# Optimization experiments

Hardware: AMD Instinct MI355X
Metric: run time of the kernel (lower is better)

## Reference

```python
import jax, jax.numpy as jnp
import numpy as np

B, N = 16, 512


def _line_coords(n):
    # Discrete Fourier slice coordinates for all mValues (center=False, ridgelet=False).
    mu = n + n // 2 if n % 2 == 0 else n + 1
    p = 2 if n % 2 == 0 else n
    m = jnp.arange(mu)           # [mu]
    k = jnp.arange(n)            # [N]
    lt = (m < n)[:, None]        # m < N branch mask, [mu, 1]
    # m < N:  row = k,                 col = (k*m) % N
    # m >= N: row = (k*p*(m-N)) % N,   col = k
    row = jnp.where(lt, k[None, :], (k[None, :] * p * (m[:, None] - n)) % n)
    col = jnp.where(lt, (k[None, :] * m[:, None]) % n, k[None, :])
    return row, col  # each [mu, N] int32


def setup_inputs() -> dict:
    key = jax.random.key(0)
    return {"image": jax.random.normal(key, (B, N, N), dtype=jnp.float32)}


def reference(image):
    b, n, _ = image.shape
    row, col = _line_coords(n)                                   # [mu, N]
    dft = jnp.fft.fft2(image.astype(jnp.complex64), norm="ortho")  # [B, N, N] c64
    slices = dft[:, row, col]                                    # gather -> [B, mu, N]
    sino = jnp.fft.ifft(slices, norm="ortho")                    # [B, mu, N] c64
    # complex sinogram returned as stacked (real, imag) float channels
    return jnp.stack([sino.real, sino.imag], axis=-1)            # [B, mu, N, 2]
```

## Files before the change

### kernel.cpp

```cpp
#include <hip/hip_runtime.h>


#define NN 512
#define MU 768
#define MASK 511
#define SCALE 0.04419417382415922f

__global__ __launch_bounds__(256) void k_init(const float* __restrict__ img,
                                              float* __restrict__ A0,
                                              float* __restrict__ B0) {
  const int bx = blockIdx.x, b = blockIdx.y;
  const float* src = img + (size_t)b * NN * NN;
  if (bx < 32) {
    __shared__ float T1[64][65], T2[64][65], T3[64][65];
    const int xt = bx & 7, wt = bx >> 3;
    const int x0 = xt * 64, w0 = wt * 64, x3 = ((xt + 4) & 7) * 64;
    for (int idx = threadIdx.x; idx < 4096; idx += 256) {
      int rr = idx >> 6, cc = idx & 63;
      T1[rr][cc] = src[(x0 + rr) * NN + w0 + cc];
      T2[rr][cc] = src[(x0 + rr) * NN + w0 + 256 + cc];
      T3[rr][cc] = src[(x3 + rr) * NN + w0 + 256 + cc];
    }
    __syncthreads();
    float* dst = A0 + (size_t)b * (512 * NN);
    for (int idx = threadIdx.x; idx < 4096; idx += 256) {
      int wl = idx >> 6, xl = idx & 63;
      float t1 = T1[xl][wl];
      dst[(size_t)(w0 + wl) * NN + x0 + xl]       = t1 + T2[xl][wl];
      dst[(size_t)(256 + w0 + wl) * NN + x0 + xl] = t1 + T3[xl][wl];
    }
  } else {
    const int w0 = (bx - 32) * 32;
    const float4* s4 = (const float4*)src;
    float4* d4 = (float4*)(B0 + (size_t)b * (256 * NN));
    for (int it = 0; it < 16; ++it) {
      int flat = it * 256 + threadIdx.x;
      int row = w0 + (flat >> 7), col = flat & 127;
      float4 u = s4[row * 128 + col], v = s4[(row + 256) * 128 + col];
      u.x += v.x; u.y += v.y; u.z += v.z; u.w += v.w;
      d4[row * 128 + col] = u;
    }
  }
}

__global__ __launch_bounds__(512, 6) void k_pass1(const float* __restrict__ A0,
                                                  const float* __restrict__ B0,
                                                  float* __restrict__ A1,
                                                  float* __restrict__ B1) {
  __shared__ float L[16 * 512];
  const int bx = blockIdx.x, b = blockIdx.y;
  const int t = threadIdx.x;
  const bool isB = bx >= 32;
  const int c = isB ? 0 : (bx >> 4);
  const int w = isB ? (bx - 32) : (bx & 15);
  const float* in = isB ? (B0 + (size_t)b * 256 * NN) : (A0 + (size_t)b * 512 * NN);
  {
    const float4* s4 = (const float4*)in;
    float4* l4 = (float4*)L;
    const int pbase = c * 256 + w;
    for (int it = 0; it < 4; ++it) {
      int flat = it * 512 + t;
      int lrow = flat >> 7, col = flat & 127;
      l4[lrow * 128 + col] = s4[(pbase + 16 * lrow) * 128 + col];
    }
  }
  __syncthreads();
  const int g = t >> 7;
  const int x4 = (t & 127) * 4;
  float* outA = A1 + (size_t)b * 512 * NN;
  float* outB = B1 + (size_t)b * 256 * NN;
  for (int jj = 0; jj < 4; ++jj) {
    const int j = jj * 4 + g;
    const int C = isB ? (2 * j) : (c + 2 * j);
    float4 acc = {0.f, 0.f, 0.f, 0.f};
#pragma unroll
    for (int bb = 0; bb < 16; ++bb) {
      int base = (x4 - C * bb * 16) & MASK;
      float4 v = *(const float4*)&L[bb * 512 + base];
      acc.x += v.x; acc.y += v.y; acc.z += v.z; acc.w += v.w;
    }
    const int orow = isB ? (j * 16 + w) : (C * 16 + w);
    float* op = isB ? outB : outA;
    *(float4*)&op[(size_t)orow * NN + x4] = acc;
  }
}

__global__ __launch_bounds__(512, 6) void k_pass2(const float* __restrict__ A1,
                                                  const float* __restrict__ B1,
                                                  float2* __restrict__ out) {
  __shared__ float L[16 * 512];
  const int bx = blockIdx.x, b = blockIdx.y;
  const int t = threadIdx.x;
  const bool isB = bx >= 32;
  const int c = isB ? 2 * (bx - 32) : bx;
  const float* in = isB ? (B1 + (size_t)b * 256 * NN + (size_t)(bx - 32) * 16 * NN)
                        : (A1 + (size_t)b * 512 * NN + (size_t)c * 16 * NN);
#pragma unroll
  for (int bb = 0; bb < 16; ++bb) {
    float v = in[bb * 512 + t];
    L[bb * 512 + ((t + c * bb) & MASK)] = v;
  }
  __syncthreads();
  const int g = t >> 7;
  const int xq = (t & 127) << 2;
  float4 acc[4];
#pragma unroll
  for (int jj = 0; jj < 4; ++jj) acc[jj] = {0.f, 0.f, 0.f, 0.f};
#pragma unroll
  for (int bb = 0; bb < 16; ++bb) {
    const float* row = L + bb * 512;
    int base = (xq - 128 * g * bb) & MASK;
    const int step = (32 * bb) & MASK;
#pragma unroll
    for (int jj = 0; jj < 4; ++jj) {
      float4 v = *(const float4*)&row[base];
      acc[jj].x += v.x; acc[jj].y += v.y; acc[jj].z += v.z; acc[jj].w += v.w;
      base = (base - step) & MASK;
    }
  }
#pragma unroll
  for (int jj = 0; jj < 4; ++jj) {
    const int j = 4 * g + jj;
    const int m = isB ? (512 + (bx - 32) + 16 * j) : (c + 32 * j);
    float2* op = out + ((size_t)b * MU + m) * NN + xq;
    float4 a = acc[jj];
    op[0] = {a.x * SCALE, 0.f};
    op[1] = {a.y * SCALE, 0.f};
    op[2] = {a.z * SCALE, 0.f};
    op[3] = {a.w * SCALE, 0.f};
  }
}

#define TM 16
#define YT 16
#define LDS_STRIDE 516
__global__ __launch_bounds__(512) void drt_main(const float* __restrict__ img,
                                                float* __restrict__ out) {
  __shared__ float rows[YT * LDS_STRIDE];
  const int b = blockIdx.y;
  const int tile = blockIdx.x;
  const int t = threadIdx.x;
  const bool caseB = (tile >= 32);
  const int a0 = caseB ? (tile - 32) * TM : tile * TM;
  const float* __restrict__ src = img + (size_t)b * (NN * NN);
  const int slope0 = caseB ? (2 * a0) : a0;
  const int dslope = caseB ? 2 : 1;
  float acc[TM];
#pragma unroll
  for (int i = 0; i < TM; ++i) acc[i] = 0.0f;
  for (int y0 = 0; y0 < NN; y0 += YT) {
    __syncthreads();
    if (caseB) {
#pragma unroll
      for (int r = 0; r < YT; ++r) rows[r * LDS_STRIDE + t] = src[(y0 + r) * NN + t];
    } else {
#pragma unroll
      for (int rep = 0; rep < YT; ++rep) {
        int idx = rep * NN + t;
        int xx = idx >> 4, cc = idx & 15;
        rows[cc * LDS_STRIDE + xx] = src[xx * NN + y0 + cc];
      }
    }
    __syncthreads();
#pragma unroll 4
    for (int r = 0; r < YT; ++r) {
      const int v = y0 + r;
      int base = t - slope0 * v;
      const int step = dslope * v;
      const float* __restrict__ rowp = rows + r * LDS_STRIDE;
#pragma unroll
      for (int i = 0; i < TM; ++i) { acc[i] += rowp[base & MASK]; base -= step; }
    }
  }
  const int m = caseB ? (NN + a0) : a0;
  float2* outp = (float2*)out;
#pragma unroll
  for (int i = 0; i < TM; ++i) {
    float2 vv; vv.x = acc[i] * SCALE; vv.y = 0.0f;
    outp[((size_t)b * MU + (m + i)) * NN + t] = vv;
  }
}

extern "C" void kernel_launch(void* const* d_in, const int* in_sizes, int n_in,
                              void* d_out, int out_size, void* d_ws, size_t ws_size,
                              hipStream_t stream) {
  const float* img = (const float*)d_in[0];
  if (ws_size < (size_t)51 * 1024 * 1024) {
    drt_main<<<dim3(48, 16), dim3(512), 0, stream>>>(img, (float*)d_out);
    return;
  }
  float* W  = (float*)d_ws;
  float* A0 = W;
  float* A1 = W + 4194304;
  float* B0 = W + 8388608;
  float* B1 = W + 10485760;

  k_init <<<dim3(40, 16), dim3(256), 0, stream>>>(img, A0, B0);
  k_pass1<<<dim3(48, 16), dim3(512), 0, stream>>>(A0, B0, A1, B1);
  k_pass2<<<dim3(48, 16), dim3(512), 0, stream>>>(A1, B1, (float2*)d_out);
}
```

Before: 108.8 us.

## Fuse three DRT passes into one persistent kernel with fp16 intermediates

Merges the init, pass1 and pass2 kernels into a single persistent launch of 768 blocks that synchronises through atomic-counter grid barriers. The intermediate A/B buffers are stored in half precision to halve workspace traffic, and the final output uses nontemporal vector stores. This removes two kernel-launch gaps and cuts intermediate memory bandwidth. In exchange it loses precision in the intermediate sums, relies on all blocks being co-resident to avoid a barrier deadlock, adds a memset and an occupancy query on the host, and drops the workspace-free fallback.

```diff
diff --git a/kernel.cpp b/kernel.cpp
--- a/kernel.cpp
+++ b/kernel.cpp
@@ -1,10 +1,177 @@
 #include <hip/hip_runtime.h>
+#include <hip/hip_fp16.h>
 
 
 #define NN 512
 #define MU 768
 #define MASK 511
 #define SCALE 0.04419417382415922f
+#define NB 768
+
+typedef float v4f __attribute__((ext_vector_type(4)));
+
+union H8 { float4 f4; __half2 h2[4]; };
+union H4 { float2 f2; __half2 h2[2]; };
+
+__device__ __forceinline__ void gridbar(unsigned* cnt, unsigned target) {
+  __syncthreads();
+  if (threadIdx.x == 0) {
+    __threadfence();
+    atomicAdd(cnt, 1u);
+    while (__atomic_load_n(cnt, __ATOMIC_ACQUIRE) < target)
+      __builtin_amdgcn_s_sleep(8);
+    __threadfence();
+  }
+  __syncthreads();
+}
+
+__global__ __launch_bounds__(512, 6) void drt_fused(
+    const float* __restrict__ img, float2* __restrict__ out,
+    __half* __restrict__ A0, __half* __restrict__ B0,
+    __half* __restrict__ A1, __half* __restrict__ B1,
+    unsigned* __restrict__ bar) {
+  __shared__ float LDS[8320];
+  const int bid = blockIdx.x;
+  const int t = threadIdx.x;
+
+  if (bid < 512) {
+    const int b = bid >> 5, tile = bid & 31;
+    const int xt = tile & 7, wt = tile >> 3;
+    const int x0 = xt * 64, w0 = wt * 64, x3 = ((xt + 4) & 7) * 64;
+    const float* src = img + (size_t)b * NN * NN;
+    float* TA = LDS;
+    float* TB = LDS + 4160;
+    for (int idx = t; idx < 4096; idx += 512) {
+      int rr = idx >> 6, cc = idx & 63;
+      TA[rr * 65 + cc] = src[(x0 + rr) * NN + w0 + cc];
+      TB[rr * 65 + cc] = src[(x0 + rr) * NN + w0 + 256 + cc];
+    }
+    __syncthreads();
+    __half2* d = (__half2*)A0 + (size_t)b * 512 * 256;
+    for (int idx = t; idx < 2048; idx += 512) {
+      int wl = idx >> 5, xp = idx & 31;
+      float a0 = TA[(2 * xp) * 65 + wl] + TB[(2 * xp) * 65 + wl];
+      float a1 = TA[(2 * xp + 1) * 65 + wl] + TB[(2 * xp + 1) * 65 + wl];
+      d[(w0 + wl) * 256 + (x0 >> 1) + xp] = __float22half2_rn(make_float2(a0, a1));
+    }
+    __syncthreads();
+    for (int idx = t; idx < 4096; idx += 512) {
+      int rr = idx >> 6, cc = idx & 63;
+      TB[rr * 65 + cc] = src[(x3 + rr) * NN + w0 + 256 + cc];
+    }
+    __syncthreads();
+    for (int idx = t; idx < 2048; idx += 512) {
+      int wl = idx >> 5, xp = idx & 31;
+      float a0 = TA[(2 * xp) * 65 + wl] + TB[(2 * xp) * 65 + wl];
+      float a1 = TA[(2 * xp + 1) * 65 + wl] + TB[(2 * xp + 1) * 65 + wl];
+      d[(256 + w0 + wl) * 256 + (x0 >> 1) + xp] = __float22half2_rn(make_float2(a0, a1));
+    }
+  } else {
+    const int v = bid - 512, b = v >> 4, unit = v & 15;
+    const int w0 = unit * 16;
+    const float2* s2 = (const float2*)(img + (size_t)b * NN * NN);
+    __half2* d = (__half2*)B0 + (size_t)b * 256 * 256;
+    for (int it = 0; it < 8; ++it) {
+      int flat = it * 512 + t;
+      int row = w0 + (flat >> 8), cp = flat & 255;
+      float2 u = s2[row * 256 + cp], vv = s2[(row + 256) * 256 + cp];
+      d[row * 256 + cp] = __float22half2_rn(make_float2(u.x + vv.x, u.y + vv.y));
+    }
+  }
+
+  gridbar(bar, NB);
+
+  {
+    const int b = bid / 48, bx = bid - b * 48;
+    const bool isB = bx >= 32;
+    const int c = isB ? 0 : (bx >> 4);
+    const int w = isB ? (bx - 32) : (bx & 15);
+    const __half* in = isB ? (B0 + (size_t)b * 256 * NN) : (A0 + (size_t)b * 512 * NN);
+    const int pbase = c * 256 + w;
+    float* L = LDS;
+    const float4* s4 = (const float4*)in;
+    for (int it = 0; it < 2; ++it) {
+      int flat = it * 512 + t;
+      int lrow = flat >> 6, ch = flat & 63;
+      H8 u; u.f4 = s4[(size_t)(pbase + 16 * lrow) * 64 + ch];
+      float2 p0 = __half22float2(u.h2[0]), p1 = __half22float2(u.h2[1]);
+      float2 p2 = __half22float2(u.h2[2]), p3 = __half22float2(u.h2[3]);
+      float4* l4 = (float4*)&L[lrow * 512 + ch * 8];
+      l4[0] = make_float4(p0.x, p0.y, p1.x, p1.y);
+      l4[1] = make_float4(p2.x, p2.y, p3.x, p3.y);
+    }
+    __syncthreads();
+    const int g = t >> 7;
+    const int x4 = (t & 127) * 4;
+    __half* outA = A1 + (size_t)b * 512 * NN;
+    __half* outB = B1 + (size_t)b * 256 * NN;
+    for (int jj = 0; jj < 4; ++jj) {
+      const int j = jj * 4 + g;
+      const int C = isB ? (2 * j) : (c + 2 * j);
+      float4 acc = {0.f, 0.f, 0.f, 0.f};
+#pragma unroll
+      for (int bb = 0; bb < 16; ++bb) {
+        int base = (x4 - C * bb * 16) & MASK;
+        float4 v = *(const float4*)&L[bb * 512 + base];
+        acc.x += v.x; acc.y += v.y; acc.z += v.z; acc.w += v.w;
+      }
+      const int orow = isB ? (j * 16 + w) : (C * 16 + w);
+      H4 h;
+      h.h2[0] = __float22half2_rn(make_float2(acc.x, acc.y));
+      h.h2[1] = __float22half2_rn(make_float2(acc.z, acc.w));
+      float2* op = (float2*)(isB ? outB : outA);
+      op[orow * 128 + (x4 >> 2)] = h.f2;
+    }
+  }
+
+  gridbar(bar, 2 * NB);
+
+  {
+    const int b = bid / 48, bx = bid - b * 48;
+    const bool isB = bx >= 32;
+    const int c = isB ? 2 * (bx - 32) : bx;
+    const __half* in = isB ? (B1 + (size_t)b * 256 * NN + (size_t)(bx - 32) * 16 * NN)
+                           : (A1 + (size_t)b * 512 * NN + (size_t)c * 16 * NN);
+    float* L = LDS;
+    const __half2* i2 = (const __half2*)in;
+    for (int it = 0; it < 8; ++it) {
+      int flat = it * 512 + t;
+      int bb = flat >> 8, p = flat & 255;
+      float2 f = __half22float2(i2[bb * 256 + p]);
+      int y0 = (2 * p + c * bb) & MASK;
+      L[bb * 512 + y0] = f.x;
+      L[bb * 512 + ((y0 + 1) & MASK)] = f.y;
+    }
+    __syncthreads();
+    const int g = t >> 7;
+    const int xq = (t & 127) << 2;
+    float4 acc[4];
+#pragma unroll
+    for (int jj = 0; jj < 4; ++jj) acc[jj] = {0.f, 0.f, 0.f, 0.f};
+#pragma unroll
+    for (int bb = 0; bb < 16; ++bb) {
+      const float* row = L + bb * 512;
+      int base = (xq - 128 * g * bb) & MASK;
+      const int step = (32 * bb) & MASK;
+#pragma unroll
+      for (int jj = 0; jj < 4; ++jj) {
+        float4 v = *(const float4*)&row[base];
+        acc[jj].x += v.x; acc[jj].y += v.y; acc[jj].z += v.z; acc[jj].w += v.w;
+        base = (base - step) & MASK;
+      }
+    }
+#pragma unroll
+    for (int jj = 0; jj < 4; ++jj) {
+      const int j = 4 * g + jj;
+      const int m = isB ? (512 + (bx - 32) + 16 * j) : (c + 32 * j);
+      v4f o1 = {acc[jj].x * SCALE, 0.f, acc[jj].y * SCALE, 0.f};
+      v4f o2 = {acc[jj].z * SCALE, 0.f, acc[jj].w * SCALE, 0.f};
+      v4f* op = (v4f*)(out + ((size_t)b * MU + m) * NN + xq);
+      __builtin_nontemporal_store(o1, op);
+      __builtin_nontemporal_store(o2, op + 1);
+    }
+  }
+}
 
 __global__ __launch_bounds__(256) void k_init(const float* __restrict__ img,
                                               float* __restrict__ A0,
@@ -43,10 +210,10 @@
   }
 }
 
-__global__ __launch_bounds__(512, 6) void k_pass1(const float* __restrict__ A0,
-                                                  const float* __restrict__ B0,
-                                                  float* __restrict__ A1,
-                                                  float* __restrict__ B1) {
+__global__ __launch_bounds__(512) void k_pass1(const float* __restrict__ A0,
+                                               const float* __restrict__ B0,
+                                               float* __restrict__ A1,
+                                               float* __restrict__ B1) {
   __shared__ float L[16 * 512];
   const int bx = blockIdx.x, b = blockIdx.y;
   const int t = threadIdx.x;
@@ -85,9 +252,9 @@
   }
 }
 
-__global__ __launch_bounds__(512, 6) void k_pass2(const float* __restrict__ A1,
-                                                  const float* __restrict__ B1,
-                                                  float2* __restrict__ out) {
+__global__ __launch_bounds__(512) void k_pass2(const float* __restrict__ A1,
+                                               const float* __restrict__ B1,
+                                               float2* __restrict__ out) {
   __shared__ float L[16 * 512];
   const int bx = blockIdx.x, b = blockIdx.y;
   const int t = threadIdx.x;
@@ -131,71 +298,34 @@
   }
 }
 
-#define TM 16
-#define YT 16
-#define LDS_STRIDE 516
-__global__ __launch_bounds__(512) void drt_main(const float* __restrict__ img,
-                                                float* __restrict__ out) {
-  __shared__ float rows[YT * LDS_STRIDE];
-  const int b = blockIdx.y;
-  const int tile = blockIdx.x;
-  const int t = threadIdx.x;
-  const bool caseB = (tile >= 32);
-  const int a0 = caseB ? (tile - 32) * TM : tile * TM;
-  const float* __restrict__ src = img + (size_t)b * (NN * NN);
-  const int slope0 = caseB ? (2 * a0) : a0;
-  const int dslope = caseB ? 2 : 1;
-  float acc[TM];
-#pragma unroll
-  for (int i = 0; i < TM; ++i) acc[i] = 0.0f;
-  for (int y0 = 0; y0 < NN; y0 += YT) {
-    __syncthreads();
-    if (caseB) {
-#pragma unroll
-      for (int r = 0; r < YT; ++r) rows[r * LDS_STRIDE + t] = src[(y0 + r) * NN + t];
-    } else {
-#pragma unroll
-      for (int rep = 0; rep < YT; ++rep) {
-        int idx = rep * NN + t;
-        int xx = idx >> 4, cc = idx & 15;
-        rows[cc * LDS_STRIDE + xx] = src[xx * NN + y0 + cc];
-      }
-    }
-    __syncthreads();
-#pragma unroll 4
-    for (int r = 0; r < YT; ++r) {
-      const int v = y0 + r;
-      int base = t - slope0 * v;
-      const int step = dslope * v;
-      const float* __restrict__ rowp = rows + r * LDS_STRIDE;
-#pragma unroll
-      for (int i = 0; i < TM; ++i) { acc[i] += rowp[base & MASK]; base -= step; }
-    }
-  }
-  const int m = caseB ? (NN + a0) : a0;
-  float2* outp = (float2*)out;
-#pragma unroll
-  for (int i = 0; i < TM; ++i) {
-    float2 vv; vv.x = acc[i] * SCALE; vv.y = 0.0f;
-    outp[((size_t)b * MU + (m + i)) * NN + t] = vv;
-  }
-}
-
 extern "C" void kernel_launch(void* const* d_in, const int* in_sizes, int n_in,
                               void* d_out, int out_size, void* d_ws, size_t ws_size,
                               hipStream_t stream) {
   const float* img = (const float*)d_in[0];
-  if (ws_size < (size_t)51 * 1024 * 1024) {
-    drt_main<<<dim3(48, 16), dim3(512), 0, stream>>>(img, (float*)d_out);
-    return;
-  }
-  float* W  = (float*)d_ws;
-  float* A0 = W;
-  float* A1 = W + 4194304;
-  float* B0 = W + 8388608;
-  float* B1 = W + 10485760;
-
-  k_init <<<dim3(40, 16), dim3(256), 0, stream>>>(img, A0, B0);
-  k_pass1<<<dim3(48, 16), dim3(512), 0, stream>>>(A0, B0, A1, B1);
-  k_pass2<<<dim3(48, 16), dim3(512), 0, stream>>>(A1, B1, (float2*)d_out);
-}
+
+  int maxb = 0;
+  (void)hipOccupancyMaxActiveBlocksPerMultiprocessor(&maxb, (const void*)drt_fused,
+                                                     512, 0);
+  const bool can_fuse = (maxb >= 3) && (ws_size >= (size_t)25165832);
+
+  if (can_fuse) {
+    char* W = (char*)d_ws;
+    __half* A0 = (__half*)(W);
+    __half* A1 = (__half*)(W + 8388608);
+    __half* B0 = (__half*)(W + 16777216);
+    __half* B1 = (__half*)(W + 20971520);
+    unsigned* bar = (unsigned*)(W + 25165824);
+    (void)hipMemsetAsync(bar, 0, 8, stream);
+    drt_fused<<<dim3(NB), dim3(512), 0, stream>>>(img, (float2*)d_out,
+                                                  A0, B0, A1, B1, bar);
+  } else if (ws_size >= (size_t)51 * 1024 * 1024) {
+    float* W  = (float*)d_ws;
+    float* A0 = W;
+    float* A1 = W + 4194304;
+    float* B0 = W + 8388608;
+    float* B1 = W + 10485760;
+    k_init <<<dim3(40, 16), dim3(256), 0, stream>>>(img, A0, B0);
+    k_pass1<<<dim3(48, 16), dim3(512), 0, stream>>>(A0, B0, A1, B1);
+    k_pass2<<<dim3(48, 16), dim3(512), 0, stream>>>(A1, B1, (float2*)d_out);
+  }
+}
```

New measurement: 108.9 us. No clear change (+0.1%).
